# Performance work log

Hardware: AMD Instinct MI355X
Metric: run time of the kernel (lower is better)

Reference implementation:

```python
import jax, jax.numpy as jnp
import numpy as np

N = 40962  # icosphere level-6 vertex count
EPS = 1e-5

def setup_inputs() -> dict:
    key = jax.random.key(0)
    ks = jax.random.split(key, 8)
    x = jax.random.normal(ks[0], (N, 3), dtype=jnp.float32)
    neigh_orders = jax.random.randint(ks[1], (N * 7,), 0, N, dtype=jnp.int32)
    s0 = 1.0 / np.sqrt(21.0)
    sm = 1.0 / np.sqrt(896.0)
    return {
        "x": x,
        "neigh_orders": neigh_orders,
        "W0": jax.random.uniform(ks[2], (21, 128), jnp.float32, -s0, s0),
        "b0": jax.random.uniform(ks[3], (128,), jnp.float32, -s0, s0),
        "g0": jnp.ones((128,), jnp.float32),
        "be0": jnp.zeros((128,), jnp.float32),
        "Wm": jax.random.uniform(ks[4], (14, 896, 128), jnp.float32, -sm, sm),
        "bm": jax.random.uniform(ks[5], (14, 128), jnp.float32, -sm, sm),
        "gm": jnp.ones((14, 128), jnp.float32),
        "bem": jnp.zeros((14, 128), jnp.float32),
        "Wl": jax.random.uniform(ks[6], (896, 36), jnp.float32, -sm, sm),
        "bl": jax.random.uniform(ks[7], (36,), jnp.float32, -sm, sm),
    }

def _bs(x, idx, W, b):
    # gather 7 fixed ring neighbors per node, flatten, dense linear
    mat = x[idx].reshape(x.shape[0], -1)  # [N, 7*in_feats]
    return mat @ W + b

def _bn_train(h, g, be):
    # BatchNorm1d in training mode: biased variance over the node/batch dim
    mu = jnp.mean(h, axis=0)
    var = jnp.var(h, axis=0)
    return g * (h - mu) * jax.lax.rsqrt(var + EPS) + be

def reference(x, neigh_orders, W0, b0, g0, be0, Wm, bm, gm, bem, Wl, bl):
    idx = neigh_orders
    h = jax.nn.relu(_bn_train(_bs(x, idx, W0, b0), g0, be0))  # [N, 128]

    def step(h, params):
        W, b, g, be = params
        h = jax.nn.relu(_bn_train(_bs(h, idx, W, b), g, be))
        return h, None

    h, _ = jax.lax.scan(step, h, (Wm, bm, gm, bem))  # 14 identical 128->128 blocks
    out = _bs(h, idx, Wl, bl)  # [N, num_classes]
    return out
```

## Files before the change

kernel.cpp:

```cpp
#include <hip/hip_runtime.h>

typedef _Float16 f16x8 __attribute__((ext_vector_type(8)));
typedef float f32x4 __attribute__((ext_vector_type(4)));

#define EPS 1e-5f

__device__ __forceinline__ short f2h(float x) {
    _Float16 h = (_Float16)x;
    union { _Float16 h; short s; } u;
    u.h = h;
    return u.s;
}

__global__ void prep_kernel(const float* __restrict__ Wm, const float* __restrict__ Wl,
                            short* __restrict__ WtM, short* __restrict__ WtF,
                            float* __restrict__ stats) {
    const long T1 = 14L * 896 * 128;
    const long T2 = 48L * 896;
    const long T3 = 15L * 256;
    long i = (long)blockIdx.x * blockDim.x + threadIdx.x;
    if (i < T1) {
        long l = i / (896 * 128);
        long r = i % (896 * 128);
        long k = r >> 7;
        long f = r & 127;
        WtM[l * 114688 + f * 896 + k] = f2h(Wm[i]);
    } else if (i < T1 + T2) {
        long j = i - T1;
        long f = j / 896;
        long k = j % 896;
        WtF[j] = (f < 36) ? f2h(Wl[k * 36 + f]) : (short)0;
    } else if (i < T1 + T2 + T3) {
        stats[i - T1 - T2] = 0.0f;
    }
}

#define L0_NB 16
__global__ __launch_bounds__(256) void layer0_kernel(
        const float* __restrict__ x, const int* __restrict__ idx,
        const float* __restrict__ W0, const float* __restrict__ b0,
        short* __restrict__ hlin, float* __restrict__ stats, int N) {
    __shared__ float sX[L0_NB * 21];
    __shared__ float sStat[256];
    const int tid = threadIdx.x;
    const int f = tid & 127;
    const int half = tid >> 7;
    float wreg[21];
#pragma unroll
    for (int k = 0; k < 21; ++k) wreg[k] = W0[k * 128 + f];
    const float bf = b0[f];
    float s = 0.f, ss = 0.f;
    const int ntiles = (N + L0_NB - 1) / L0_NB;
    for (int t = blockIdx.x; t < ntiles; t += gridDim.x) {
        const int n0 = t * L0_NB;
        __syncthreads();
        for (int i = tid; i < L0_NB * 21; i += 256) {
            int ni = i / 21;
            int k = i - ni * 21;
            int j = k / 3;
            int c = k - j * 3;
            int n = n0 + ni;
            if (n >= N) n = N - 1;
            sX[i] = x[(long)idx[n * 7 + j] * 3 + c];
        }
        __syncthreads();
#pragma unroll
        for (int ni = 0; ni < 8; ++ni) {
            int node = n0 + half * 8 + ni;
            if (node >= N) break;
            float acc = bf;
#pragma unroll
            for (int k = 0; k < 21; ++k)
                acc = fmaf(sX[(half * 8 + ni) * 21 + k], wreg[k], acc);
            hlin[(long)node * 128 + f] = f2h(acc);
            s += acc;
            ss += acc * acc;
        }
    }
    __syncthreads();
    if (half == 1) { sStat[f] = s; sStat[128 + f] = ss; }
    __syncthreads();
    if (half == 0) {
        atomicAdd(&stats[f], s + sStat[f]);
        atomicAdd(&stats[128 + f], ss + sStat[128 + f]);
    }
}

__global__ __launch_bounds__(256, 4) void gemm_mid_kernel(
        const short* __restrict__ hprev, const int* __restrict__ idx,
        const short* __restrict__ Wt, const float* __restrict__ bvec,
        const float* __restrict__ g, const float* __restrict__ be,
        const float* __restrict__ statsIn,
        short* __restrict__ hlin, float* __restrict__ statsOut,
        int N, float invN) {
    __shared__ short sA[64 * 136];
    __shared__ short sB[64 * 136];
    __shared__ float sAux[256];

    const int tid = threadIdx.x;
    const int wave = tid >> 6;
    const int lane = tid & 63;
    const int quad = lane >> 4;
    const int l16 = lane & 15;
    const int wm = wave & 1;
    const int wf = wave >> 1;
    const int tile = blockIdx.x >> 1;
    const int fg = blockIdx.x & 1;
    const int m0 = tile * 64;
    const int f0 = fg * 64;
    const int t16 = tid >> 4;
    const int fb = (tid & 15) * 8;

    if (tid < 128) {
        float mu = statsIn[tid] * invN;
        float var = statsIn[128 + tid] * invN - mu * mu;
        float rs = rsqrtf(var + EPS);
        float sc = g[tid] * rs;
        sAux[tid] = sc;
        sAux[128 + tid] = be[tid] - mu * sc;
    }
    __syncthreads();
    float scR[8], shR[8];
#pragma unroll
    for (int e = 0; e < 8; ++e) {
        scR[e] = sAux[fb + e];
        shR[e] = sAux[128 + fb + e];
    }

    f32x4 acc[2][2];
#pragma unroll
    for (int ni = 0; ni < 2; ++ni) {
        float bv0 = bvec[f0 + wf * 32 + ni * 16 + l16];
#pragma unroll
        for (int mi = 0; mi < 2; ++mi) {
            acc[mi][ni][0] = bv0; acc[mi][ni][1] = bv0; acc[mi][ni][2] = bv0; acc[mi][ni][3] = bv0;
        }
    }

    f16x8 av[4];
    f16x8 bv[4];

    auto issueA = [&](int j) {
#pragma unroll
        for (int it = 0; it < 4; ++it) {
            int nl = t16 + it * 16;
            int n = m0 + nl;
            n = (n < N) ? n : (N - 1);
            long row = idx[n * 7 + j];
            av[it] = *(const f16x8*)&hprev[row * 128 + fb];
        }
    };
    auto issueB = [&](int j) {
#pragma unroll
        for (int it = 0; it < 4; ++it) {
            int ff = f0 + t16 + it * 16;
            bv[it] = *(const f16x8*)&Wt[(long)ff * 896 + j * 128 + fb];
        }
    };
    auto writeA = [&]() {
#pragma unroll
        for (int it = 0; it < 4; ++it) {
            int nl = t16 + it * 16;
            f16x8 hv = av[it];
            union { short sh8[8]; f16x8 v; } u;
#pragma unroll
            for (int e = 0; e < 8; ++e) {
                float v = (float)hv[e];
                u.sh8[e] = f2h(fmaxf(fmaf(v, scR[e], shR[e]), 0.f));
            }
            *(f16x8*)&sA[nl * 136 + fb] = u.v;
        }
    };
    auto writeB = [&]() {
#pragma unroll
        for (int it = 0; it < 4; ++it) {
            int ffl = t16 + it * 16;
            *(f16x8*)&sB[ffl * 136 + fb] = bv[it];
        }
    };

    issueB(0);
    issueA(0);

    for (int j = 0; j < 7; ++j) {
        __syncthreads();
        writeB();
        writeA();
        if (j < 6) {
            issueB(j + 1);
            issueA(j + 1);
        }
        __syncthreads();
#pragma unroll
        for (int k0 = 0; k0 < 128; k0 += 32) {
            f16x8 a[2], b[2];
#pragma unroll
            for (int mi = 0; mi < 2; ++mi)
                a[mi] = *(const f16x8*)&sA[(wm * 32 + mi * 16 + l16) * 136 + k0 + quad * 8];
#pragma unroll
            for (int ni = 0; ni < 2; ++ni)
                b[ni] = *(const f16x8*)&sB[(wf * 32 + ni * 16 + l16) * 136 + k0 + quad * 8];
#pragma unroll
            for (int mi = 0; mi < 2; ++mi)
#pragma unroll
                for (int ni = 0; ni < 2; ++ni)
                    acc[mi][ni] = __builtin_amdgcn_mfma_f32_16x16x32_f16(a[mi], b[ni], acc[mi][ni], 0, 0, 0);
        }
    }

    __syncthreads();
    if (tid < 128) sAux[tid] = 0.f;
    __syncthreads();
#pragma unroll
    for (int ni = 0; ni < 2; ++ni) {
        int lf = wf * 32 + ni * 16 + l16;
        float s = 0.f, ss = 0.f;
#pragma unroll
        for (int mi = 0; mi < 2; ++mi) {
#pragma unroll
            for (int r = 0; r < 4; ++r) {
                int node = m0 + wm * 32 + mi * 16 + quad * 4 + r;
                float v = acc[mi][ni][r];
                if (node < N) {
                    hlin[(long)node * 128 + f0 + lf] = f2h(v);
                    s += v;
                    ss += v * v;
                }
            }
        }
        atomicAdd(&sAux[lf], s);
        atomicAdd(&sAux[64 + lf], ss);
    }
    __syncthreads();
    if (tid < 64) {
        atomicAdd(&statsOut[f0 + tid], sAux[tid]);
        atomicAdd(&statsOut[128 + f0 + tid], sAux[64 + tid]);
    }
}

__global__ __launch_bounds__(256) void gemm_final_kernel(
        const short* __restrict__ hprev, const int* __restrict__ idx,
        const short* __restrict__ WtF, const float* __restrict__ bl,
        const float* __restrict__ g, const float* __restrict__ be,
        const float* __restrict__ statsIn,
        float* __restrict__ out, int N, float invN) {
    __shared__ short sA[64 * 136];
    __shared__ short sB[48 * 136];
    __shared__ float sAux[256];

    const int tid = threadIdx.x;
    const int wave = tid >> 6;
    const int lane = tid & 63;
    const int quad = lane >> 4;
    const int l16 = lane & 15;
    const int m0 = blockIdx.x * 64;
    const int t16 = tid >> 4;
    const int fb = (tid & 15) * 8;

    if (tid < 128) {
        float mu = statsIn[tid] * invN;
        float var = statsIn[128 + tid] * invN - mu * mu;
        float rs = rsqrtf(var + EPS);
        float sc = g[tid] * rs;
        sAux[tid] = sc;
        sAux[128 + tid] = be[tid] - mu * sc;
    }
    __syncthreads();
    float scR[8], shR[8];
#pragma unroll
    for (int e = 0; e < 8; ++e) {
        scR[e] = sAux[fb + e];
        shR[e] = sAux[128 + fb + e];
    }

    f32x4 acc[3];
#pragma unroll
    for (int ni = 0; ni < 3; ++ni) {
        int feat = ni * 16 + l16;
        float bv0 = (feat < 36) ? bl[feat] : 0.f;
        acc[ni][0] = bv0; acc[ni][1] = bv0; acc[ni][2] = bv0; acc[ni][3] = bv0;
    }

    f16x8 av[4];
    f16x8 bv[3];

    auto issueA = [&](int j) {
#pragma unroll
        for (int it = 0; it < 4; ++it) {
            int nl = t16 + it * 16;
            int n = m0 + nl;
            n = (n < N) ? n : (N - 1);
            long row = idx[n * 7 + j];
            av[it] = *(const f16x8*)&hprev[row * 128 + fb];
        }
    };
    auto issueB = [&](int j) {
#pragma unroll
        for (int it = 0; it < 3; ++it) {
            int ff = t16 + it * 16;
            bv[it] = *(const f16x8*)&WtF[(long)ff * 896 + j * 128 + fb];
        }
    };
    auto writeA = [&]() {
#pragma unroll
        for (int it = 0; it < 4; ++it) {
            int nl = t16 + it * 16;
            f16x8 hv = av[it];
            union { short sh8[8]; f16x8 v; } u;
#pragma unroll
            for (int e = 0; e < 8; ++e) {
                float v = (float)hv[e];
                u.sh8[e] = f2h(fmaxf(fmaf(v, scR[e], shR[e]), 0.f));
            }
            *(f16x8*)&sA[nl * 136 + fb] = u.v;
        }
    };
    auto writeB = [&]() {
#pragma unroll
        for (int it = 0; it < 3; ++it) {
            int ff = t16 + it * 16;
            *(f16x8*)&sB[ff * 136 + fb] = bv[it];
        }
    };

    issueB(0);
    issueA(0);

    for (int j = 0; j < 7; ++j) {
        __syncthreads();
        writeB();
        writeA();
        if (j < 6) {
            issueB(j + 1);
            issueA(j + 1);
        }
        __syncthreads();
#pragma unroll
        for (int k0 = 0; k0 < 128; k0 += 32) {
            f16x8 a = *(const f16x8*)&sA[(wave * 16 + l16) * 136 + k0 + quad * 8];
            f16x8 b[3];
#pragma unroll
            for (int ni = 0; ni < 3; ++ni)
                b[ni] = *(const f16x8*)&sB[(ni * 16 + l16) * 136 + k0 + quad * 8];
#pragma unroll
            for (int ni = 0; ni < 3; ++ni)
                acc[ni] = __builtin_amdgcn_mfma_f32_16x16x32_f16(a, b[ni], acc[ni], 0, 0, 0);
        }
    }

#pragma unroll
    for (int ni = 0; ni < 3; ++ni) {
        int feat = ni * 16 + l16;
        if (feat < 36) {
#pragma unroll
            for (int r = 0; r < 4; ++r) {
                int node = m0 + wave * 16 + quad * 4 + r;
                if (node < N) out[(long)node * 36 + feat] = acc[ni][r];
            }
        }
    }
}

extern "C" void kernel_launch(void* const* d_in, const int* in_sizes, int n_in,
                              void* d_out, int out_size, void* d_ws, size_t ws_size,
                              hipStream_t stream) {
    const float* x   = (const float*)d_in[0];
    const int*   idx = (const int*)d_in[1];
    const float* W0  = (const float*)d_in[2];
    const float* b0  = (const float*)d_in[3];
    const float* g0  = (const float*)d_in[4];
    const float* be0 = (const float*)d_in[5];
    const float* Wm  = (const float*)d_in[6];
    const float* bm  = (const float*)d_in[7];
    const float* gm  = (const float*)d_in[8];
    const float* bem = (const float*)d_in[9];
    const float* Wl  = (const float*)d_in[10];
    const float* bl  = (const float*)d_in[11];
    float* out = (float*)d_out;

    const int N = in_sizes[0] / 3;
    const float invN = 1.0f / (float)N;

    char* ws = (char*)d_ws;
    size_t off = 0;
    auto alloc = [&](size_t bytes) -> void* {
        void* p = ws + off;
        off = (off + bytes + 255) & ~(size_t)255;
        return p;
    };
    short* WtM   = (short*)alloc(14UL * 128 * 896 * 2);
    short* WtF   = (short*)alloc(48UL * 896 * 2);
    float* stats = (float*)alloc(15UL * 256 * 4);
    short* hlinA = (short*)alloc((size_t)N * 128 * 2);
    short* hlinB = (short*)alloc((size_t)N * 128 * 2);

    {
        long total = 14L * 896 * 128 + 48L * 896 + 15L * 256;
        int blocks = (int)((total + 255) / 256);
        prep_kernel<<<blocks, 256, 0, stream>>>(Wm, Wl, WtM, WtF, stats);
    }

    const int ntiles0 = (N + L0_NB - 1) / L0_NB;
    layer0_kernel<<<ntiles0, 256, 0, stream>>>(x, idx, W0, b0, hlinA, stats, N);

    const int gblocks_mid = ((N + 63) / 64) * 2;
    short* hin = hlinA;
    short* hout = hlinB;
    const float* gPrev = g0;
    const float* bePrev = be0;
    for (int L = 0; L < 14; ++L) {
        gemm_mid_kernel<<<gblocks_mid, 256, 0, stream>>>(
            hin, idx, WtM + (size_t)L * 128 * 896, bm + L * 128,
            gPrev, bePrev, stats + L * 256,
            hout, stats + (L + 1) * 256, N, invN);
        gPrev = gm + L * 128;
        bePrev = bem + L * 128;
        short* t = hin; hin = hout; hout = t;
    }

    const int gblocks_fin = (N + 63) / 64;
    gemm_final_kernel<<<gblocks_fin, 256, 0, stream>>>(
        hin, idx, WtF, bl, gm + 13 * 128, bem + 13 * 128, stats + 14 * 256,
        out, N, invN);
}
```

Measured before the change: 641.3 us.

## Prefetch layer-0 neighbor gathers into registers and use persistent grid

```diff
diff --git a/kernel.cpp b/kernel.cpp
--- a/kernel.cpp
+++ b/kernel.cpp
@@ -51,18 +51,35 @@
     const float bf = b0[f];
     float s = 0.f, ss = 0.f;
     const int ntiles = (N + L0_NB - 1) / L0_NB;
-    for (int t = blockIdx.x; t < ntiles; t += gridDim.x) {
+    const int gs = gridDim.x;
+
+    const int e0 = tid;
+    const int ni0 = e0 / 21, k0e = e0 - ni0 * 21;
+    const int j0 = k0e / 3, c0 = k0e - j0 * 3;
+    const int e1 = tid + 256;
+    const int ni1 = e1 / 21, k1e = e1 - ni1 * 21;
+    const int j1 = k1e / 3, c1 = k1e - j1 * 3;
+
+    auto issueX = [&](int t, float& a0, float& a1) {
+        if (t >= ntiles) return;
+        const int base = t * L0_NB;
+        int n = base + ni0; if (n >= N) n = N - 1;
+        a0 = x[(long)idx[n * 7 + j0] * 3 + c0];
+        if (tid < 80) {
+            int n2 = base + ni1; if (n2 >= N) n2 = N - 1;
+            a1 = x[(long)idx[n2 * 7 + j1] * 3 + c1];
+        }
+    };
+
+    float cx0 = 0.f, cx1 = 0.f, nx0 = 0.f, nx1 = 0.f;
+    issueX(blockIdx.x, cx0, cx1);
+
+    for (int t = blockIdx.x; t < ntiles; t += gs) {
         const int n0 = t * L0_NB;
         __syncthreads();
-        for (int i = tid; i < L0_NB * 21; i += 256) {
-            int ni = i / 21;
-            int k = i - ni * 21;
-            int j = k / 3;
-            int c = k - j * 3;
-            int n = n0 + ni;
-            if (n >= N) n = N - 1;
-            sX[i] = x[(long)idx[n * 7 + j] * 3 + c];
-        }
+        sX[e0] = cx0;
+        if (tid < 80) sX[e1] = cx1;
+        issueX(t + gs, nx0, nx1);
         __syncthreads();
 #pragma unroll
         for (int ni = 0; ni < 8; ++ni) {
@@ -76,6 +93,7 @@
             s += acc;
             ss += acc * acc;
         }
+        cx0 = nx0; cx1 = nx1;
     }
     __syncthreads();
     if (half == 1) { sStat[f] = s; sStat[128 + f] = ss; }
@@ -400,8 +418,7 @@
         prep_kernel<<<blocks, 256, 0, stream>>>(Wm, Wl, WtM, WtF, stats);
     }
 
-    const int ntiles0 = (N + L0_NB - 1) / L0_NB;
-    layer0_kernel<<<ntiles0, 256, 0, stream>>>(x, idx, W0, b0, hlinA, stats, N);
+    layer0_kernel<<<1280, 256, 0, stream>>>(x, idx, W0, b0, hlinA, stats, N);
 
     const int gblocks_mid = ((N + 63) / 64) * 2;
     short* hin = hlinA;
```

New measurement: 607.2 us. 5.3% less time.
